# Optimization experiments

Hardware: AMD Instinct MI355X
Metric: run time of the kernel (lower is better)

Reference implementation:

```python
import jax, jax.numpy as jnp
import numpy as np

B, S, E = 4, 2048, 512
H, D = 8, 64  # n_head, attn_dim


def setup_inputs() -> dict:
    key = jax.random.key(0)
    ks = jax.random.split(key, 12)
    scale = 0.02
    return {
        "input_q": jax.random.normal(ks[0], (B, S, E), dtype=jnp.float32),
        "input_k": jax.random.normal(ks[1], (B, S, E), dtype=jnp.float32),
        "input_v": jax.random.normal(ks[2], (B, S, E), dtype=jnp.float32),
        "mask": jax.random.randint(ks[3], (B, S, S), 0, 2, dtype=jnp.int32),
        "wq": jax.random.normal(ks[4], (E, H * D), dtype=jnp.float32) * scale,
        "bq": jnp.zeros((H * D,), dtype=jnp.float32),
        "wk": jax.random.normal(ks[5], (E, H * D), dtype=jnp.float32) * scale,
        "bk": jnp.zeros((H * D,), dtype=jnp.float32),
        "wv": jax.random.normal(ks[6], (E, H * D), dtype=jnp.float32) * scale,
        "bv": jnp.zeros((H * D,), dtype=jnp.float32),
        "wo": jax.random.normal(ks[7], (H * D, E), dtype=jnp.float32) * scale,
        "bo": jnp.zeros((E,), dtype=jnp.float32),
    }


def reference(input_q, input_k, input_v, mask, wq, bq, wk, bk, wv, bv, wo, bo):
    b, lq, _ = input_q.shape
    lk = input_k.shape[1]
    # projections -> [b, len, H, D] -> [b, H, len, D]
    q = (input_q @ wq + bq).reshape(b, lq, H, D).transpose(0, 2, 1, 3)
    k = (input_k @ wk + bk).reshape(b, lk, H, D).transpose(0, 2, 1, 3)
    v = (input_v @ wv + bv).reshape(b, lk, H, D).transpose(0, 2, 1, 3)
    # raw scores [b, H, lq, lk]
    score = jnp.einsum("bhqd,bhkd->bhqk", q, k)
    # NOTE: original masks with -1e9 BEFORE dividing by sqrt(attn_dim)
    score = jnp.where(mask[:, None, :, :] == 0, jnp.float32(-1e9), score)
    attn = jax.nn.softmax(score / jnp.sqrt(jnp.float32(D)), axis=-1)
    out = jnp.einsum("bhqk,bhkd->bqhd", attn, v).reshape(b, lq, H * D)
    return out @ wo + bo
```

## Files before the change

### kernel.cpp

```cpp
#include <hip/hip_runtime.h>
#include <hip/hip_bf16.h>
#include <hip/hip_fp16.h>
#include <stdint.h>

#define Bc 4
#define Sc 2048
#define Ec 512
#define Hc 8
#define Dc 64
#define HDc 512

typedef __attribute__((ext_vector_type(8))) short bf16x8;
typedef __attribute__((ext_vector_type(4))) _Float16 f16x4;
typedef __attribute__((ext_vector_type(4))) float f32x4;
typedef unsigned int u32;

__device__ __forceinline__ unsigned short f2bf(float x) {
    union { float f; unsigned u; } v; v.f = x;
    unsigned r = v.u + 0x7FFFu + ((v.u >> 16) & 1u);
    return (unsigned short)(r >> 16);
}

__device__ __forceinline__ unsigned pkbf2(float a, float b) {
    float2 f; f.x = a; f.y = b;
    __hip_bfloat162 h = __float22bfloat162_rn(f);
    union { __hip_bfloat162 h2; unsigned u; } u; u.h2 = h;
    return u.u;
}

__device__ __forceinline__ unsigned short f2h(float x) {
    return __half_as_ushort(__float2half_rn(x));
}

__device__ __forceinline__ unsigned pkh2(float a, float b) {
    union { __half2 h2; unsigned u; } u;
    u.h2 = __floats2half2_rn(a, b);
    return u.u;
}

__device__ __forceinline__ uint4 pack8(float4 a, float4 b) {
    uint4 v;
    v.x = pkbf2(a.x, a.y); v.y = pkbf2(a.z, a.w);
    v.z = pkbf2(b.x, b.y); v.w = pkbf2(b.z, b.w);
    return v;
}

__device__ __forceinline__ void gload_lds(const void* g, void* l) {
    __builtin_amdgcn_global_load_lds(
        (const __attribute__((address_space(1))) u32*)g,
        (__attribute__((address_space(3))) u32*)l,
        16, 0, 0);
}

__global__ __launch_bounds__(256) void prep(
    const int* __restrict__ mask, unsigned long long* __restrict__ bits,
    const float* __restrict__ W0, const float* __restrict__ W1,
    const float* __restrict__ W2, const float* __restrict__ W3,
    unsigned short* __restrict__ Wt)
{
    const int blk = blockIdx.x;
    __shared__ float t[64][65];
    if (blk < 256) {
        const int z = blk >> 6;
        const float* W = z == 0 ? W0 : (z == 1 ? W1 : (z == 2 ? W2 : W3));
        unsigned short* O = Wt + (size_t)z * Ec * HDc;
        const int k0 = ((blk >> 3) & 7) * 64, n0 = (blk & 7) * 64;
#pragma unroll
        for (int i = 0; i < 16; i++) {
            int idx = threadIdx.x + 256 * i;
            int kr = idx >> 6, nc = idx & 63;
            t[nc][kr] = W[(size_t)(k0 + kr) * HDc + n0 + nc];
        }
        __syncthreads();
#pragma unroll
        for (int i = 0; i < 16; i++) {
            int idx = threadIdx.x + 256 * i;
            int nr = idx >> 6, kc = idx & 63;
            O[(size_t)(n0 + nr) * Ec + k0 + kc] = f2bf(t[nr][kc]);
        }
    } else {
        const int lane = threadIdx.x & 63;
        int wave = ((blk - 256) * 256 + (int)threadIdx.x) >> 6;
        const int nwaves = (2048 * 256) >> 6;
        const int nwords = (Bc * Sc * Sc) / 64;
        for (int w = wave; w < nwords; w += nwaves) {
            int m = mask[(size_t)w * 64 + lane];
            unsigned long long b = __ballot(m != 0);
            if (lane == 0) bits[w] = b;
        }
    }
}

__global__ __launch_bounds__(256) void proj_gemm(
    const float* __restrict__ Xq, const float* __restrict__ Xk, const float* __restrict__ Xv,
    const unsigned short* __restrict__ Wt,
    const float* __restrict__ bq, const float* __restrict__ bk, const float* __restrict__ bv,
    unsigned short* __restrict__ Oq, unsigned short* __restrict__ Ok,
    unsigned short* __restrict__ Vt)
{
    const int z = blockIdx.z;
    const float* X = z == 0 ? Xq : (z == 1 ? Xk : Xv);
    const unsigned short* Bt = Wt + (size_t)z * Ec * HDc;
    const float* bias = z == 0 ? bq : (z == 1 ? bk : bv);

    const int n0 = blockIdx.x * 128;
    const int m0 = blockIdx.y * 128;
    const int tid = threadIdx.x, lane = tid & 63, w = tid >> 6;
    const int c = lane & 15, quad = lane >> 4;
    const int wm = w & 1, wn = w >> 1;

    __shared__ unsigned short As[128 * 64];
    __shared__ unsigned short Bs[128 * 64];

    f32x4 acc[4][4];
#pragma unroll
    for (int i = 0; i < 4; i++)
#pragma unroll
        for (int j = 0; j < 4; j++) acc[i][j] = (f32x4){0.f, 0.f, 0.f, 0.f};

    for (int k0 = 0; k0 < Ec; k0 += 64) {
        __syncthreads();
#pragma unroll
        for (int jj = 0; jj < 4; jj++) {
            int rb = w * 32 + jj * 8;
            int row = rb + (lane >> 3);
            int dg = (lane & 7) ^ (row & 7);
            gload_lds(Bt + (size_t)(n0 + row) * Ec + k0 + dg * 8, &Bs[rb * 64]);
        }
#pragma unroll
        for (int s = 0; s < 4; s++) {
            int idx = tid + 256 * s;
            int row = idx >> 3, kp = idx & 7;
            int dg = kp ^ (row & 7);
            const float* src = X + (size_t)(m0 + row) * Ec + k0 + dg * 8;
            float4 fa = *(const float4*)src;
            float4 fb = *(const float4*)(src + 4);
            *(uint4*)&As[row * 64 + kp * 8] = pack8(fa, fb);
        }
        __syncthreads();
#pragma unroll
        for (int ks = 0; ks < 2; ks++) {
            int kg = ks * 4 + quad;
            bf16x8 af[4], bfr[4];
#pragma unroll
            for (int mt = 0; mt < 4; mt++) {
                int row = wm * 64 + mt * 16 + c;
                af[mt] = *(const bf16x8*)&As[row * 64 + ((kg ^ (row & 7)) * 8)];
            }
#pragma unroll
            for (int nt = 0; nt < 4; nt++) {
                int row = wn * 64 + nt * 16 + c;
                bfr[nt] = *(const bf16x8*)&Bs[row * 64 + ((kg ^ (row & 7)) * 8)];
            }
            if (z < 2) {
#pragma unroll
                for (int mt = 0; mt < 4; mt++)
#pragma unroll
                    for (int nt = 0; nt < 4; nt++)
                        acc[mt][nt] = __builtin_amdgcn_mfma_f32_16x16x32_bf16(af[mt], bfr[nt], acc[mt][nt], 0, 0, 0);
            } else {
#pragma unroll
                for (int mt = 0; mt < 4; mt++)
#pragma unroll
                    for (int nt = 0; nt < 4; nt++)
                        acc[mt][nt] = __builtin_amdgcn_mfma_f32_16x16x32_bf16(bfr[nt], af[mt], acc[mt][nt], 0, 0, 0);
            }
        }
    }

    if (z < 2) {
        unsigned short* O = z == 0 ? Oq : Ok;
        const float qs = z == 0 ? 0.125f : 1.0f;
#pragma unroll
        for (int mt = 0; mt < 4; mt++)
#pragma unroll
            for (int r = 0; r < 4; r++) {
                int gm = m0 + wm * 64 + mt * 16 + quad * 4 + r;
#pragma unroll
                for (int nt = 0; nt < 4; nt++) {
                    int gn = n0 + wn * 64 + nt * 16 + c;
                    O[(size_t)gm * HDc + gn] = f2bf((acc[mt][nt][r] + bias[gn]) * qs);
                }
            }
    } else {
#pragma unroll
        for (int mt = 0; mt < 4; mt++) {
            int gm = m0 + wm * 64 + mt * 16 + c;
            int bb = gm >> 11, sPos = gm & (Sc - 1);
#pragma unroll
            for (int nt = 0; nt < 4; nt++)
#pragma unroll
                for (int r = 0; r < 4; r++) {
                    int ng = n0 + wn * 64 + nt * 16 + quad * 4 + r;
                    int hh = ng >> 6, d = ng & 63;
                    Vt[((size_t)(bb * Hc + hh) * Dc + d) * Sc + sPos] = f2h(acc[mt][nt][r] + bias[ng]);
                }
        }
    }
}

__global__ __launch_bounds__(256, 4) void attn_kernel(
    const unsigned short* __restrict__ Qb, const unsigned short* __restrict__ Kb,
    const unsigned short* __restrict__ Vt, const unsigned long long* __restrict__ Mb,
    unsigned short* __restrict__ Ob)
{
    const int qt = blockIdx.x;
    const int h  = blockIdx.y;
    const int b  = blockIdx.z;
    const int q0 = qt * 64;
    const int tid = threadIdx.x, lane = tid & 63, w = tid >> 6;
    const int c = lane & 15, quad = lane >> 4;

    __shared__ unsigned short Ks[2][64 * 64];
    __shared__ unsigned short Vs[2][64 * 64];

    const int qg = q0 + w * 16 + c;
    const size_t qoff = ((size_t)b * Sc + qg) * HDc + h * Dc;

    bf16x8 qf[2];
    qf[0] = *(const bf16x8*)(Qb + qoff + quad * 8);
    qf[1] = *(const bf16x8*)(Qb + qoff + 32 + quad * 8);

    const unsigned long long* mr = Mb + ((size_t)b * Sc + qg) * (Sc / 64);
    const size_t kbase = ((size_t)b * Sc) * HDc + h * Dc;
    const size_t vbase = ((size_t)(b * Hc + h)) * Dc * Sc;

    f32x4 o[4], osum;
#pragma unroll
    for (int i = 0; i < 4; i++) o[i] = (f32x4){0.f, 0.f, 0.f, 0.f};
    osum = (f32x4){0.f, 0.f, 0.f, 0.f};

    const f16x4 ones = {(_Float16)1.0f, (_Float16)1.0f, (_Float16)1.0f, (_Float16)1.0f};

    auto stage = [&](int kt, int buf) {
#pragma unroll
        for (int j = 0; j < 2; j++) {
            int rb = w * 16 + j * 8;
            int row = rb + (lane >> 3);
            int dg = (lane & 7) ^ (row & 7);
            gload_lds(Kb + kbase + (size_t)(kt * 64 + row) * HDc + dg * 8, &Ks[buf][rb * 64]);
            gload_lds(Vt + vbase + (size_t)row * Sc + kt * 64 + dg * 8, &Vs[buf][rb * 64]);
        }
    };

    stage(0, 0);
    for (int kt = 0; kt < Sc / 64; kt++) {
        const int cur = kt & 1;
        unsigned long long mw = mr[kt];
        __syncthreads();
        if (kt + 1 < Sc / 64) stage(kt + 1, cur ^ 1);

        f32x4 s[4];
#pragma unroll
        for (int nt = 0; nt < 4; nt++) s[nt] = (f32x4){0.f, 0.f, 0.f, 0.f};
#pragma unroll
        for (int ks = 0; ks < 2; ks++) {
            int kg = ks * 4 + quad;
#pragma unroll
            for (int nt = 0; nt < 4; nt++) {
                int t = nt * 16 + c;
                bf16x8 a = *(const bf16x8*)&Ks[cur][t * 64 + ((kg ^ (t & 7)) * 8)];
                s[nt] = __builtin_amdgcn_mfma_f32_16x16x32_bf16(a, qf[ks], s[nt], 0, 0, 0);
            }
        }

        u32 mlo = (u32)(mw) >> (quad * 4);
        u32 mhi = (u32)(mw >> 32) >> (quad * 4);
        f16x4 pb[4];
#pragma unroll
        for (int nt = 0; nt < 4; nt++) {
            u32 msrc = (nt < 2) ? mlo : mhi;
            float p[4];
#pragma unroll
            for (int r = 0; r < 4; r++) {
                const int sh = (nt & 1) * 16 + r;
                int keep = ((int)(msrc << (31 - sh))) >> 31;
                float e = __expf(s[nt][r]);
                p[r] = __int_as_float(__float_as_int(e) & keep);
            }
            union { unsigned u[2]; f16x4 v; } pk;
            pk.u[0] = pkh2(p[0], p[1]);
            pk.u[1] = pkh2(p[2], p[3]);
            pb[nt] = pk.v;
        }

#pragma unroll
        for (int ntb = 0; ntb < 4; ntb++) {
#pragma unroll
            for (int dt = 0; dt < 4; dt++) {
                int d = dt * 16 + c;
                const f16x4 a = *(const f16x4*)&Vs[cur][d * 64 +
                    (((ntb * 2 + (quad >> 1)) ^ (d & 7)) * 8) + ((quad & 1) * 4)];
                o[dt] = __builtin_amdgcn_mfma_f32_16x16x16f16(a, pb[ntb], o[dt], 0, 0, 0);
            }
            osum = __builtin_amdgcn_mfma_f32_16x16x16f16(ones, pb[ntb], osum, 0, 0, 0);
        }
    }

    const float inv = 1.0f / osum[0];

#pragma unroll
    for (int nt = 0; nt < 4; nt++) {
        uint2 pk;
        pk.x = pkbf2(o[nt][0] * inv, o[nt][1] * inv);
        pk.y = pkbf2(o[nt][2] * inv, o[nt][3] * inv);
        *(uint2*)(Ob + qoff + nt * 16 + quad * 4) = pk;
    }
}

__global__ __launch_bounds__(256) void out_gemm(
    const unsigned short* __restrict__ Ab, const unsigned short* __restrict__ Bt,
    const float* __restrict__ bias, float* __restrict__ Out)
{
    const int n0 = blockIdx.x * 128;
    const int m0 = blockIdx.y * 64;
    const int tid = threadIdx.x, lane = tid & 63, w = tid >> 6;
    const int c = lane & 15, quad = lane >> 4;
    const int wm = w & 1, wn = w >> 1;

    __shared__ unsigned short As[64 * 64];
    __shared__ unsigned short Bs[128 * 64];

    f32x4 acc[2][4];
#pragma unroll
    for (int i = 0; i < 2; i++)
#pragma unroll
        for (int j = 0; j < 4; j++) acc[i][j] = (f32x4){0.f, 0.f, 0.f, 0.f};

    for (int k0 = 0; k0 < HDc; k0 += 64) {
        __syncthreads();
#pragma unroll
        for (int jj = 0; jj < 4; jj++) {
            int rb = w * 32 + jj * 8;
            int row = rb + (lane >> 3);
            int dg = (lane & 7) ^ (row & 7);
            gload_lds(Bt + (size_t)(n0 + row) * Ec + k0 + dg * 8, &Bs[rb * 64]);
        }
#pragma unroll
        for (int jj = 0; jj < 2; jj++) {
            int rb = w * 16 + jj * 8;
            int row = rb + (lane >> 3);
            int dg = (lane & 7) ^ (row & 7);
            gload_lds(Ab + (size_t)(m0 + row) * HDc + k0 + dg * 8, &As[rb * 64]);
        }
        __syncthreads();
#pragma unroll
        for (int ks = 0; ks < 2; ks++) {
            int kg = ks * 4 + quad;
            bf16x8 af[2], bfr[4];
#pragma unroll
            for (int mt = 0; mt < 2; mt++) {
                int row = wm * 32 + mt * 16 + c;
                af[mt] = *(const bf16x8*)&As[row * 64 + ((kg ^ (row & 7)) * 8)];
            }
#pragma unroll
            for (int nt = 0; nt < 4; nt++) {
                int row = wn * 64 + nt * 16 + c;
                bfr[nt] = *(const bf16x8*)&Bs[row * 64 + ((kg ^ (row & 7)) * 8)];
            }
#pragma unroll
            for (int mt = 0; mt < 2; mt++)
#pragma unroll
                for (int nt = 0; nt < 4; nt++)
                    acc[mt][nt] = __builtin_amdgcn_mfma_f32_16x16x32_bf16(af[mt], bfr[nt], acc[mt][nt], 0, 0, 0);
        }
    }
#pragma unroll
    for (int mt = 0; mt < 2; mt++)
#pragma unroll
        for (int r = 0; r < 4; r++) {
            int gm = m0 + wm * 32 + mt * 16 + quad * 4 + r;
#pragma unroll
            for (int nt = 0; nt < 4; nt++) {
                int gn = n0 + wn * 64 + nt * 16 + c;
                Out[(size_t)gm * Ec + gn] = acc[mt][nt][r] + bias[gn];
            }
        }
}

extern "C" void kernel_launch(void* const* d_in, const int* in_sizes, int n_in,
                              void* d_out, int out_size, void* d_ws, size_t ws_size,
                              hipStream_t stream)
{
    const float* xq = (const float*)d_in[0];
    const float* xk = (const float*)d_in[1];
    const float* xv = (const float*)d_in[2];
    const int* mask = (const int*)d_in[3];
    const float* wq = (const float*)d_in[4];
    const float* bq = (const float*)d_in[5];
    const float* wk = (const float*)d_in[6];
    const float* bk = (const float*)d_in[7];
    const float* wv = (const float*)d_in[8];
    const float* bv = (const float*)d_in[9];
    const float* wo = (const float*)d_in[10];
    const float* bo = (const float*)d_in[11];
    float* out = (float*)d_out;

    char* ws = (char*)d_ws;
    unsigned short* qb = (unsigned short*)(ws + (size_t)0 * 1024 * 1024);
    unsigned short* kb = (unsigned short*)(ws + (size_t)8 * 1024 * 1024);
    unsigned short* vt = (unsigned short*)(ws + (size_t)16 * 1024 * 1024);
    unsigned short* ab = (unsigned short*)(ws + (size_t)24 * 1024 * 1024);
    unsigned long long* mb = (unsigned long long*)(ws + (size_t)32 * 1024 * 1024);
    unsigned short* wt = (unsigned short*)(ws + (size_t)48 * 1024 * 1024);

    hipLaunchKernelGGL(prep, dim3(2304), dim3(256), 0, stream,
                       mask, mb, wq, wk, wv, wo, wt);

    const size_t WSZ = (size_t)Ec * HDc;
    hipLaunchKernelGGL(proj_gemm, dim3(4, 64, 3), dim3(256), 0, stream,
                       xq, xk, xv, wt, bq, bk, bv, qb, kb, vt);

    hipLaunchKernelGGL(attn_kernel, dim3(32, 8, 4), dim3(256), 0, stream,
                       qb, kb, vt, mb, ab);

    hipLaunchKernelGGL(out_gemm, dim3(4, 128), dim3(256), 0, stream,
                       ab, wt + 3 * WSZ, bo, out);
}
```

Measured before the change: 287.7 us.

## Pre-convert activations to bf16 and permute V layout for wider LDS reads

The prep kernel gains extra blocks that convert the fp32 Q/K/V inputs to bf16 in a workspace, so proj_gemm can stage A tiles with async global-to-LDS loads instead of loading and converting in registers. The V-transpose epilogue writes sequence positions in a permuted order, which lets the attention kernel read 8 fp16 values per LDS load and feed two MFMAs from each read. The cost is an extra full-activation read and write pass, plus the bf16 activation buffer sharing its workspace region with the attention output.

```diff
diff --git a/kernel.cpp b/kernel.cpp
--- a/kernel.cpp
+++ b/kernel.cpp
@@ -12,6 +12,7 @@
 
 typedef __attribute__((ext_vector_type(8))) short bf16x8;
 typedef __attribute__((ext_vector_type(4))) _Float16 f16x4;
+typedef __attribute__((ext_vector_type(8))) _Float16 f16x8;
 typedef __attribute__((ext_vector_type(4))) float f32x4;
 typedef unsigned int u32;
 
@@ -52,11 +53,17 @@
         16, 0, 0);
 }
 
+__device__ __forceinline__ int vperm(int mt, int c) {
+    return ((c >> 2) << 4) + ((mt >> 1) << 3) + ((mt & 1) << 2) + (c & 3);
+}
+
 __global__ __launch_bounds__(256) void prep(
     const int* __restrict__ mask, unsigned long long* __restrict__ bits,
     const float* __restrict__ W0, const float* __restrict__ W1,
     const float* __restrict__ W2, const float* __restrict__ W3,
-    unsigned short* __restrict__ Wt)
+    unsigned short* __restrict__ Wt,
+    const float* __restrict__ Xq, const float* __restrict__ Xk,
+    const float* __restrict__ Xv, unsigned short* __restrict__ Xb)
 {
     const int blk = blockIdx.x;
     __shared__ float t[64][65];
@@ -78,7 +85,7 @@
             int nr = idx >> 6, kc = idx & 63;
             O[(size_t)(n0 + nr) * Ec + k0 + kc] = f2bf(t[nr][kc]);
         }
-    } else {
+    } else if (blk < 2304) {
         const int lane = threadIdx.x & 63;
         int wave = ((blk - 256) * 256 + (int)threadIdx.x) >> 6;
         const int nwaves = (2048 * 256) >> 6;
@@ -88,18 +95,25 @@
             unsigned long long b = __ballot(m != 0);
             if (lane == 0) bits[w] = b;
         }
+    } else {
+        const int zi = blk - 2304;
+        const int z = zi >> 11, wi = zi & 2047;
+        const float* X = z == 0 ? Xq : (z == 1 ? Xk : Xv);
+        const size_t off = ((size_t)wi * 256 + threadIdx.x) * 8;
+        const float4* p = (const float4*)(X + off);
+        float4 f0 = p[0], f1 = p[1];
+        *(uint4*)(Xb + (size_t)z * 4194304 + off) = pack8(f0, f1);
     }
 }
 
 __global__ __launch_bounds__(256) void proj_gemm(
-    const float* __restrict__ Xq, const float* __restrict__ Xk, const float* __restrict__ Xv,
-    const unsigned short* __restrict__ Wt,
+    const unsigned short* __restrict__ Xb, const unsigned short* __restrict__ Wt,
     const float* __restrict__ bq, const float* __restrict__ bk, const float* __restrict__ bv,
     unsigned short* __restrict__ Oq, unsigned short* __restrict__ Ok,
     unsigned short* __restrict__ Vt)
 {
     const int z = blockIdx.z;
-    const float* X = z == 0 ? Xq : (z == 1 ? Xk : Xv);
+    const unsigned short* Xz = Xb + (size_t)z * 4194304;
     const unsigned short* Bt = Wt + (size_t)z * Ec * HDc;
     const float* bias = z == 0 ? bq : (z == 1 ? bk : bv);
 
@@ -126,16 +140,7 @@
             int row = rb + (lane >> 3);
             int dg = (lane & 7) ^ (row & 7);
             gload_lds(Bt + (size_t)(n0 + row) * Ec + k0 + dg * 8, &Bs[rb * 64]);
-        }
-#pragma unroll
-        for (int s = 0; s < 4; s++) {
-            int idx = tid + 256 * s;
-            int row = idx >> 3, kp = idx & 7;
-            int dg = kp ^ (row & 7);
-            const float* src = X + (size_t)(m0 + row) * Ec + k0 + dg * 8;
-            float4 fa = *(const float4*)src;
-            float4 fb = *(const float4*)(src + 4);
-            *(uint4*)&As[row * 64 + kp * 8] = pack8(fa, fb);
+            gload_lds(Xz + (size_t)(m0 + row) * Ec + k0 + dg * 8, &As[rb * 64]);
         }
         __syncthreads();
 #pragma unroll
@@ -187,13 +192,14 @@
         for (int mt = 0; mt < 4; mt++) {
             int gm = m0 + wm * 64 + mt * 16 + c;
             int bb = gm >> 11, sPos = gm & (Sc - 1);
+            int tbase = (sPos & ~63) + vperm(mt, c);
 #pragma unroll
             for (int nt = 0; nt < 4; nt++)
 #pragma unroll
                 for (int r = 0; r < 4; r++) {
                     int ng = n0 + wn * 64 + nt * 16 + quad * 4 + r;
                     int hh = ng >> 6, d = ng & 63;
-                    Vt[((size_t)(bb * Hc + hh) * Dc + d) * Sc + sPos] = f2h(acc[mt][nt][r] + bias[ng]);
+                    Vt[((size_t)(bb * Hc + hh) * Dc + d) * Sc + tbase] = f2h(acc[mt][nt][r] + bias[ng]);
                 }
         }
     }
@@ -285,26 +291,28 @@
         }
 
 #pragma unroll
-        for (int ntb = 0; ntb < 4; ntb++) {
+        for (int a = 0; a < 2; a++) {
 #pragma unroll
             for (int dt = 0; dt < 4; dt++) {
                 int d = dt * 16 + c;
-                const f16x4 a = *(const f16x4*)&Vs[cur][d * 64 +
-                    (((ntb * 2 + (quad >> 1)) ^ (d & 7)) * 8) + ((quad & 1) * 4)];
-                o[dt] = __builtin_amdgcn_mfma_f32_16x16x16f16(a, pb[ntb], o[dt], 0, 0, 0);
-            }
-            osum = __builtin_amdgcn_mfma_f32_16x16x16f16(ones, pb[ntb], osum, 0, 0, 0);
+                union { f16x8 v8; f16x4 v4[2]; } vv;
+                vv.v8 = *(const f16x8*)&Vs[cur][d * 64 + (((quad * 2 + a) ^ (d & 7)) * 8)];
+                o[dt] = __builtin_amdgcn_mfma_f32_16x16x16f16(vv.v4[0], pb[2*a],   o[dt], 0, 0, 0);
+                o[dt] = __builtin_amdgcn_mfma_f32_16x16x16f16(vv.v4[1], pb[2*a+1], o[dt], 0, 0, 0);
+            }
+            osum = __builtin_amdgcn_mfma_f32_16x16x16f16(ones, pb[2*a],   osum, 0, 0, 0);
+            osum = __builtin_amdgcn_mfma_f32_16x16x16f16(ones, pb[2*a+1], osum, 0, 0, 0);
         }
     }
 
     const float inv = 1.0f / osum[0];
 
 #pragma unroll
-    for (int nt = 0; nt < 4; nt++) {
+    for (int dt = 0; dt < 4; dt++) {
         uint2 pk;
-        pk.x = pkbf2(o[nt][0] * inv, o[nt][1] * inv);
-        pk.y = pkbf2(o[nt][2] * inv, o[nt][3] * inv);
-        *(uint2*)(Ob + qoff + nt * 16 + quad * 4) = pk;
+        pk.x = pkbf2(o[dt][0] * inv, o[dt][1] * inv);
+        pk.y = pkbf2(o[dt][2] * inv, o[dt][3] * inv);
+        *(uint2*)(Ob + qoff + dt * 16 + quad * 4) = pk;
     }
 }
 
@@ -397,23 +405,24 @@
     float* out = (float*)d_out;
 
     char* ws = (char*)d_ws;
-    unsigned short* qb = (unsigned short*)(ws + (size_t)0 * 1024 * 1024);
-    unsigned short* kb = (unsigned short*)(ws + (size_t)8 * 1024 * 1024);
-    unsigned short* vt = (unsigned short*)(ws + (size_t)16 * 1024 * 1024);
-    unsigned short* ab = (unsigned short*)(ws + (size_t)24 * 1024 * 1024);
-    unsigned long long* mb = (unsigned long long*)(ws + (size_t)32 * 1024 * 1024);
-    unsigned short* wt = (unsigned short*)(ws + (size_t)48 * 1024 * 1024);
-
-    hipLaunchKernelGGL(prep, dim3(2304), dim3(256), 0, stream,
-                       mask, mb, wq, wk, wv, wo, wt);
-
-    const size_t WSZ = (size_t)Ec * HDc;
+    const size_t MB = 1024 * 1024;
+    unsigned short* qb = (unsigned short*)(ws + 0 * MB);
+    unsigned short* kb = (unsigned short*)(ws + 8 * MB);
+    unsigned short* vt = (unsigned short*)(ws + 16 * MB);
+    unsigned short* xb = (unsigned short*)(ws + 24 * MB);
+    unsigned short* ab = (unsigned short*)(ws + 24 * MB);
+    unsigned long long* mb = (unsigned long long*)(ws + 48 * MB);
+    unsigned short* wt = (unsigned short*)(ws + 50 * MB);
+
+    hipLaunchKernelGGL(prep, dim3(8448), dim3(256), 0, stream,
+                       mask, mb, wq, wk, wv, wo, wt, xq, xk, xv, xb);
+
     hipLaunchKernelGGL(proj_gemm, dim3(4, 64, 3), dim3(256), 0, stream,
-                       xq, xk, xv, wt, bq, bk, bv, qb, kb, vt);
+                       xb, wt, bq, bk, bv, qb, kb, vt);
 
     hipLaunchKernelGGL(attn_kernel, dim3(32, 8, 4), dim3(256), 0, stream,
                        qb, kb, vt, mb, ab);
 
     hipLaunchKernelGGL(out_gemm, dim3(4, 128), dim3(256), 0, stream,
-                       ab, wt + 3 * WSZ, bo, out);
-}
+                       ab, wt + 3 * (size_t)Ec * HDc, bo, out);
+}
```

Result: faster. 270.7 us (-5.9%).
